# Kernel optimization log

Hardware: AMD Instinct MI355X
Metric: run time of the kernel (lower is better)

Reference implementation:

```python
import jax, jax.numpy as jnp
import numpy as np

EPS = float(np.finfo(np.float64).eps)  # matches np.finfo(float).eps in the torch code
NUM_SHARED, IN_DIM, NUM_OUT_CAPS, OUT_DIM = 32, 8, 10, 16
ROUTE_NUM = 3


def setup_inputs() -> dict:
    key = jax.random.key(0)
    k1, k2, k3 = jax.random.split(key, 3)
    bs, H, W = 256, 6, 6
    x = jax.random.normal(k1, (bs, NUM_SHARED * IN_DIM, H, W), jnp.float32)
    # grouped 1x1 conv weight, reshaped per group: (num_shared, num_out_caps*out_dim, in_dim)
    W_weight = jax.random.normal(k2, (NUM_SHARED, NUM_OUT_CAPS * OUT_DIM, IN_DIM), jnp.float32) * 0.05
    W_bias = jax.random.normal(k3, (NUM_SHARED * NUM_OUT_CAPS * OUT_DIM,), jnp.float32) * 0.05
    return {"x": x, "W_weight": W_weight, "W_bias": W_bias}


def reference(x, W_weight, W_bias):
    bs, C, H, Wd = x.shape
    G, KD, in_dim = W_weight.shape
    J, D = NUM_OUT_CAPS, OUT_DIM
    # grouped 1x1 conv == per-group matmul over channels
    xg = x.reshape(bs, G, in_dim, H * Wd)                     # b g i s
    pred = jnp.einsum('gki,bgis->bgks', W_weight, xg)
    pred = pred + W_bias.reshape(G, KD, 1)
    pred = pred.reshape(bs, G, J, D, H, Wd)
    pred = jnp.transpose(pred, (0, 2, 3, 1, 4, 5)).reshape(bs, J, D, G * H * Wd)  # b j d i
    I = G * H * Wd

    # dynamic routing
    b = jnp.zeros((bs, J, I), pred.dtype)
    v = None
    for it in range(ROUTE_NUM):
        c = jax.nn.softmax(b, axis=2)                          # b j i
        s = jnp.einsum('bjdi,bji->bjd', pred, c)               # b j d
        norm = jnp.linalg.norm(s, axis=2)                      # b j
        n2 = norm * norm
        coeff2 = (n2 / (1.0 + n2)) / (norm + EPS)              # squash, 'paper' manner
        v = s * coeff2[..., None]
        if it < ROUTE_NUM - 1:
            b = b + jnp.einsum('bjd,bjdi->bji', v, pred)
    return v
```

## Files before the change

kernel.cpp:

```cpp
#include <hip/hip_runtime.h>
#include <math.h>


#define G_    32
#define J_    10
#define D_    16
#define NT_   128
#define GSW_  148

__device__ __forceinline__ float dpp_add_x1(float v) {
    const int s = __builtin_amdgcn_update_dpp(0, __float_as_int(v), 0xB1, 0xF, 0xF, true);
    return v + __int_as_float(s);
}
__device__ __forceinline__ float dpp_add_x2(float v) {
    const int s = __builtin_amdgcn_update_dpp(0, __float_as_int(v), 0x4E, 0xF, 0xF, true);
    return v + __int_as_float(s);
}
__device__ __forceinline__ float dpp_x1(float v) {
    return __int_as_float(__builtin_amdgcn_update_dpp(0, __float_as_int(v), 0xB1, 0xF, 0xF, true));
}
__device__ __forceinline__ float dpp_x2(float v) {
    return __int_as_float(__builtin_amdgcn_update_dpp(0, __float_as_int(v), 0x4E, 0xF, 0xF, true));
}

__global__ __launch_bounds__(NT_) void caps_route_kernel(
    const float* __restrict__ x,
    const float* __restrict__ Wt,
    const float* __restrict__ bias,
    float* __restrict__ out)
{
    const int B = blockIdx.x, nwg = gridDim.x;
    const int bj = ((nwg & 7) == 0) ? (B & 7) * (nwg >> 3) + (B >> 3) : B;
    const int b = bj / J_, j = bj - b * J_;
    const int t = threadIdx.x;
    const int lane = t & 63, wid = t >> 6;
    const int g = t >> 2, c = t & 3;

    __shared__ float Wk[G_ * GSW_];
    __shared__ __align__(16) float swl[2][2][D_];
    __shared__ float esw[2][2];

    float xv[8][9];
    {
        const float* xb = x + (size_t)b * 9216 + (size_t)g * 288 + 4 * c;
        #pragma unroll
        for (int k = 0; k < 8; ++k) {
            const float4 a0 = *(const float4*)(xb + k * 36);
            const float4 a1 = *(const float4*)(xb + k * 36 + 16);
            xv[k][0] = a0.x; xv[k][1] = a0.y; xv[k][2] = a0.z; xv[k][3] = a0.w;
            xv[k][4] = a1.x; xv[k][5] = a1.y; xv[k][6] = a1.z; xv[k][7] = a1.w;
            xv[k][8] = xb[k * 36 + 32 - 3 * c];
        }
    }

    #pragma unroll
    for (int rr = 0; rr < 4; ++rr) {
        const int idx = t + rr * NT_;
        const int gg = idx >> 4, d = idx & 15;
        const float* src = Wt + (size_t)gg * 1280 + j * 128 + d * 8;
        const float4 a0 = *(const float4*)(src);
        const float4 a1 = *(const float4*)(src + 4);
        float* dst = Wk + gg * GSW_ + d;
        dst[0]   = a0.x; dst[16]  = a0.y; dst[32]  = a0.z; dst[48]  = a0.w;
        dst[64]  = a1.x; dst[80]  = a1.y; dst[96]  = a1.z; dst[112] = a1.w;
        dst[128] = bias[gg * 160 + j * 16 + d];
    }
    __syncthreads();

    float b_loc[9] = {0.f,0.f,0.f,0.f,0.f,0.f,0.f,0.f,0.f};
    const float EPS = 2.220446049250313e-16f;

    #pragma unroll 1
    for (int it = 0; it < 3; ++it) {
        const int kb = it & 1;

        float yp[8] = {0.f,0.f,0.f,0.f,0.f,0.f,0.f,0.f};
        float esum = 0.f;
        if (it == 0) {
            #pragma unroll
            for (int q = 0; q < 9; ++q) {
                #pragma unroll
                for (int k = 0; k < 8; ++k) yp[k] += xv[k][q];
            }
        } else {
            #pragma unroll
            for (int q = 0; q < 9; ++q) {
                const float e = __expf(b_loc[q]);
                esum += e;
                #pragma unroll
                for (int k = 0; k < 8; ++k) yp[k] += e * xv[k][q];
            }
        }
        #pragma unroll
        for (int k = 0; k < 8; ++k) {
            yp[k] = dpp_add_x1(yp[k]);
            yp[k] = dpp_add_x2(yp[k]);
        }
        if (it > 0) { esum = dpp_add_x1(esum); esum = dpp_add_x2(esum); }
        const float cg = (it == 0) ? 36.f : esum;

        float part[4];
        const float* wg = Wk + g * GSW_ + 4 * c;
        {
            const float4 wb = *(const float4*)(wg + 128);
            part[0] = wb.x * cg; part[1] = wb.y * cg;
            part[2] = wb.z * cg; part[3] = wb.w * cg;
            #pragma unroll
            for (int k = 0; k < 8; ++k) {
                const float4 wv = *(const float4*)(wg + k * 16);
                part[0] += wv.x * yp[k]; part[1] += wv.y * yp[k];
                part[2] += wv.z * yp[k]; part[3] += wv.w * yp[k];
            }
        }
        #pragma unroll
        for (int off = 4; off <= 32; off <<= 1) {
            #pragma unroll
            for (int m = 0; m < 4; ++m) part[m] += __shfl_xor(part[m], off);
            if (it > 0) esum += __shfl_xor(esum, off);
        }
        if (lane < 4) {
            float4 pw; pw.x = part[0]; pw.y = part[1]; pw.z = part[2]; pw.w = part[3];
            *(float4*)(&swl[kb][wid][4 * lane]) = pw;
            if (lane == 0) esw[kb][wid] = esum;
        }
        __syncthreads();

        const float denom = (it == 0) ? 1152.f : (esw[kb][0] + esw[kb][1]);

        if (it < 2) {
            float ssq = 0.f, ua = 0.f, ub = 0.f, u8v = 0.f;
            const float* wgc = Wk + g * GSW_;
            #pragma unroll
            for (int m = 0; m < 4; ++m) {
                const float4 sa = ((const float4*)swl[kb][0])[m];
                const float4 sb = ((const float4*)swl[kb][1])[m];
                float4 s4; s4.x = sa.x + sb.x; s4.y = sa.y + sb.y;
                           s4.z = sa.z + sb.z; s4.w = sa.w + sb.w;
                ssq += s4.x * s4.x + s4.y * s4.y + s4.z * s4.z + s4.w * s4.w;
                const float* wa = wgc + c * 16 + 4 * m;
                const float* wb = wgc + (c + 4) * 16 + 4 * m;
                const float* w8 = wgc + 128 + 4 * m;
                ua  += s4.x * wa[0] + s4.y * wa[1] + s4.z * wa[2] + s4.w * wa[3];
                ub  += s4.x * wb[0] + s4.y * wb[1] + s4.z * wb[2] + s4.w * wb[3];
                u8v += s4.x * w8[0] + s4.y * w8[1] + s4.z * w8[2] + s4.w * w8[3];
            }
            const float alpha = 1.f / denom;
            const float n2    = ssq * alpha * alpha;
            const float nrm   = sqrtf(n2);
            const float coeff = (n2 / (1.f + n2)) / (nrm + EPS);
            const float beta  = alpha * coeff;
            ua *= beta; ub *= beta; u8v *= beta;

            const float p1a = dpp_x1(ua);
            const float p1b = dpp_x1(ub);
            const bool  o1  = (c & 1) != 0;
            const float v0 = o1 ? p1a : ua;
            const float v1 = o1 ? ua  : p1a;
            const float v4 = o1 ? p1b : ub;
            const float v5 = o1 ? ub  : p1b;
            const float q0 = dpp_x2(v0);
            const float q1 = dpp_x2(v1);
            const float q4 = dpp_x2(v4);
            const float q5 = dpp_x2(v5);
            const bool  o2 = (c & 2) != 0;
            float uk[8];
            uk[0] = o2 ? q0 : v0;  uk[1] = o2 ? q1 : v1;
            uk[2] = o2 ? v0 : q0;  uk[3] = o2 ? v1 : q1;
            uk[4] = o2 ? q4 : v4;  uk[5] = o2 ? q5 : v5;
            uk[6] = o2 ? v4 : q4;  uk[7] = o2 ? v5 : q5;
            #pragma unroll
            for (int q = 0; q < 9; ++q) {
                float acc = u8v;
                #pragma unroll
                for (int k = 0; k < 8; ++k) acc += uk[k] * xv[k][q];
                b_loc[q] += acc;
            }
        } else {
            float ssq = 0.f;
            #pragma unroll
            for (int m = 0; m < 4; ++m) {
                const float4 sa = ((const float4*)swl[kb][0])[m];
                const float4 sb = ((const float4*)swl[kb][1])[m];
                const float sx = sa.x + sb.x, sy = sa.y + sb.y;
                const float sz = sa.z + sb.z, sw = sa.w + sb.w;
                ssq += sx * sx + sy * sy + sz * sz + sw * sw;
            }
            const float alpha = 1.f / denom;
            const float n2    = ssq * alpha * alpha;
            const float nrm   = sqrtf(n2);
            const float coeff = (n2 / (1.f + n2)) / (nrm + EPS);
            const float beta  = alpha * coeff;
            if (t < D_) {
                const float sd = swl[kb][0][t] + swl[kb][1][t];
                out[(size_t)bj * D_ + t] = sd * beta;
            }
        }
    }
}

extern "C" void kernel_launch(void* const* d_in, const int* in_sizes, int n_in,
                              void* d_out, int out_size, void* d_ws, size_t ws_size,
                              hipStream_t stream) {
    const float* x    = (const float*)d_in[0];
    const float* Wt   = (const float*)d_in[1];
    const float* bias = (const float*)d_in[2];
    float* out        = (float*)d_out;

    const int bs = in_sizes[0] / 9216;
    dim3 grid(bs * J_);
    dim3 block(NT_);
    caps_route_kernel<<<grid, block, 0, stream>>>(x, Wt, bias, out);
}
```

Measured before the change: 25.18 us.

## Keep per-thread weight slice in registers instead of staging in shared memory

Each thread now loads only its own 4x8 weight slice and 4 bias values straight into registers. This removes the shared-memory weight tile, its transposed staging writes and the initial __syncthreads. The back-projection of the squashed vector is rebuilt as per-thread partial dot products reduced over the 4 lanes of a group with DPP adds, replacing the earlier shared reads and DPP/select shuffles. The cost is about 36 more VGPRs per thread alongside the large x register array, which may lower occupancy.

Result: slower. 30.88 us (+22.6%).

```diff
diff --git a/kernel.cpp b/kernel.cpp
--- a/kernel.cpp
+++ b/kernel.cpp
@@ -6,7 +6,6 @@
 #define J_    10
 #define D_    16
 #define NT_   128
-#define GSW_  148
 
 __device__ __forceinline__ float dpp_add_x1(float v) {
     const int s = __builtin_amdgcn_update_dpp(0, __float_as_int(v), 0xB1, 0xF, 0xF, true);
@@ -15,12 +14,6 @@
 __device__ __forceinline__ float dpp_add_x2(float v) {
     const int s = __builtin_amdgcn_update_dpp(0, __float_as_int(v), 0x4E, 0xF, 0xF, true);
     return v + __int_as_float(s);
-}
-__device__ __forceinline__ float dpp_x1(float v) {
-    return __int_as_float(__builtin_amdgcn_update_dpp(0, __float_as_int(v), 0xB1, 0xF, 0xF, true));
-}
-__device__ __forceinline__ float dpp_x2(float v) {
-    return __int_as_float(__builtin_amdgcn_update_dpp(0, __float_as_int(v), 0x4E, 0xF, 0xF, true));
 }
 
 __global__ __launch_bounds__(NT_) void caps_route_kernel(
@@ -36,9 +29,23 @@
     const int lane = t & 63, wid = t >> 6;
     const int g = t >> 2, c = t & 3;
 
-    __shared__ float Wk[G_ * GSW_];
     __shared__ __align__(16) float swl[2][2][D_];
     __shared__ float esw[2][2];
+
+    float Wreg[4][8];
+    float br[4];
+    {
+        const float* wsrc = Wt + (size_t)g * 1280 + j * 128 + (4 * c) * 8;
+        #pragma unroll
+        for (int m = 0; m < 4; ++m) {
+            const float4 a0 = *(const float4*)(wsrc + m * 8);
+            const float4 a1 = *(const float4*)(wsrc + m * 8 + 4);
+            Wreg[m][0] = a0.x; Wreg[m][1] = a0.y; Wreg[m][2] = a0.z; Wreg[m][3] = a0.w;
+            Wreg[m][4] = a1.x; Wreg[m][5] = a1.y; Wreg[m][6] = a1.z; Wreg[m][7] = a1.w;
+        }
+        const float4 bb = *(const float4*)(bias + (size_t)g * 160 + j * 16 + 4 * c);
+        br[0] = bb.x; br[1] = bb.y; br[2] = bb.z; br[3] = bb.w;
+    }
 
     float xv[8][9];
     {
@@ -52,20 +59,6 @@
             xv[k][8] = xb[k * 36 + 32 - 3 * c];
         }
     }
-
-    #pragma unroll
-    for (int rr = 0; rr < 4; ++rr) {
-        const int idx = t + rr * NT_;
-        const int gg = idx >> 4, d = idx & 15;
-        const float* src = Wt + (size_t)gg * 1280 + j * 128 + d * 8;
-        const float4 a0 = *(const float4*)(src);
-        const float4 a1 = *(const float4*)(src + 4);
-        float* dst = Wk + gg * GSW_ + d;
-        dst[0]   = a0.x; dst[16]  = a0.y; dst[32]  = a0.z; dst[48]  = a0.w;
-        dst[64]  = a1.x; dst[80]  = a1.y; dst[96]  = a1.z; dst[112] = a1.w;
-        dst[128] = bias[gg * 160 + j * 16 + d];
-    }
-    __syncthreads();
 
     float b_loc[9] = {0.f,0.f,0.f,0.f,0.f,0.f,0.f,0.f,0.f};
     const float EPS = 2.220446049250313e-16f;
@@ -100,17 +93,12 @@
         const float cg = (it == 0) ? 36.f : esum;
 
         float part[4];
-        const float* wg = Wk + g * GSW_ + 4 * c;
-        {
-            const float4 wb = *(const float4*)(wg + 128);
-            part[0] = wb.x * cg; part[1] = wb.y * cg;
-            part[2] = wb.z * cg; part[3] = wb.w * cg;
+        #pragma unroll
+        for (int m = 0; m < 4; ++m) {
+            float p = br[m] * cg;
             #pragma unroll
-            for (int k = 0; k < 8; ++k) {
-                const float4 wv = *(const float4*)(wg + k * 16);
-                part[0] += wv.x * yp[k]; part[1] += wv.y * yp[k];
-                part[2] += wv.z * yp[k]; part[3] += wv.w * yp[k];
-            }
+            for (int k = 0; k < 8; ++k) p += Wreg[m][k] * yp[k];
+            part[m] = p;
         }
         #pragma unroll
         for (int off = 4; off <= 32; off <<= 1) {
@@ -127,69 +115,45 @@
 
         const float denom = (it == 0) ? 1152.f : (esw[kb][0] + esw[kb][1]);
 
+        const float4 sa = *(const float4*)(&swl[kb][0][4 * c]);
+        const float4 sb = *(const float4*)(&swl[kb][1][4 * c]);
+        float s4[4];
+        s4[0] = sa.x + sb.x; s4[1] = sa.y + sb.y;
+        s4[2] = sa.z + sb.z; s4[3] = sa.w + sb.w;
+
+        float ssq = s4[0]*s4[0] + s4[1]*s4[1] + s4[2]*s4[2] + s4[3]*s4[3];
+        ssq = dpp_add_x1(ssq);
+        ssq = dpp_add_x2(ssq);
+
+        const float alpha = 1.f / denom;
+        const float n2    = ssq * alpha * alpha;
+        const float nrm   = sqrtf(n2);
+        const float coeff = (n2 / (1.f + n2)) / (nrm + EPS);
+        const float beta  = alpha * coeff;
+
         if (it < 2) {
-            float ssq = 0.f, ua = 0.f, ub = 0.f, u8v = 0.f;
-            const float* wgc = Wk + g * GSW_;
+            const float t0 = s4[0] * beta, t1 = s4[1] * beta;
+            const float t2 = s4[2] * beta, t3 = s4[3] * beta;
+            float uk[8];
             #pragma unroll
-            for (int m = 0; m < 4; ++m) {
-                const float4 sa = ((const float4*)swl[kb][0])[m];
-                const float4 sb = ((const float4*)swl[kb][1])[m];
-                float4 s4; s4.x = sa.x + sb.x; s4.y = sa.y + sb.y;
-                           s4.z = sa.z + sb.z; s4.w = sa.w + sb.w;
-                ssq += s4.x * s4.x + s4.y * s4.y + s4.z * s4.z + s4.w * s4.w;
-                const float* wa = wgc + c * 16 + 4 * m;
-                const float* wb = wgc + (c + 4) * 16 + 4 * m;
-                const float* w8 = wgc + 128 + 4 * m;
-                ua  += s4.x * wa[0] + s4.y * wa[1] + s4.z * wa[2] + s4.w * wa[3];
-                ub  += s4.x * wb[0] + s4.y * wb[1] + s4.z * wb[2] + s4.w * wb[3];
-                u8v += s4.x * w8[0] + s4.y * w8[1] + s4.z * w8[2] + s4.w * w8[3];
+            for (int k = 0; k < 8; ++k) {
+                float uu = t0 * Wreg[0][k] + t1 * Wreg[1][k]
+                         + t2 * Wreg[2][k] + t3 * Wreg[3][k];
+                uu = dpp_add_x1(uu);
+                uk[k] = dpp_add_x2(uu);
             }
-            const float alpha = 1.f / denom;
-            const float n2    = ssq * alpha * alpha;
-            const float nrm   = sqrtf(n2);
-            const float coeff = (n2 / (1.f + n2)) / (nrm + EPS);
-            const float beta  = alpha * coeff;
-            ua *= beta; ub *= beta; u8v *= beta;
+            float u8 = t0 * br[0] + t1 * br[1] + t2 * br[2] + t3 * br[3];
+            u8 = dpp_add_x1(u8);
+            u8 = dpp_add_x2(u8);
 
-            const float p1a = dpp_x1(ua);
-            const float p1b = dpp_x1(ub);
-            const bool  o1  = (c & 1) != 0;
-            const float v0 = o1 ? p1a : ua;
-            const float v1 = o1 ? ua  : p1a;
-            const float v4 = o1 ? p1b : ub;
-            const float v5 = o1 ? ub  : p1b;
-            const float q0 = dpp_x2(v0);
-            const float q1 = dpp_x2(v1);
-            const float q4 = dpp_x2(v4);
-            const float q5 = dpp_x2(v5);
-            const bool  o2 = (c & 2) != 0;
-            float uk[8];
-            uk[0] = o2 ? q0 : v0;  uk[1] = o2 ? q1 : v1;
-            uk[2] = o2 ? v0 : q0;  uk[3] = o2 ? v1 : q1;
-            uk[4] = o2 ? q4 : v4;  uk[5] = o2 ? q5 : v5;
-            uk[6] = o2 ? v4 : q4;  uk[7] = o2 ? v5 : q5;
             #pragma unroll
             for (int q = 0; q < 9; ++q) {
-                float acc = u8v;
+                float acc = u8;
                 #pragma unroll
                 for (int k = 0; k < 8; ++k) acc += uk[k] * xv[k][q];
                 b_loc[q] += acc;
             }
         } else {
-            float ssq = 0.f;
-            #pragma unroll
-            for (int m = 0; m < 4; ++m) {
-                const float4 sa = ((const float4*)swl[kb][0])[m];
-                const float4 sb = ((const float4*)swl[kb][1])[m];
-                const float sx = sa.x + sb.x, sy = sa.y + sb.y;
-                const float sz = sa.z + sb.z, sw = sa.w + sb.w;
-                ssq += sx * sx + sy * sy + sz * sz + sw * sw;
-            }
-            const float alpha = 1.f / denom;
-            const float n2    = ssq * alpha * alpha;
-            const float nrm   = sqrtf(n2);
-            const float coeff = (n2 / (1.f + n2)) / (nrm + EPS);
-            const float beta  = alpha * coeff;
             if (t < D_) {
                 const float sd = swl[kb][0][t] + swl[kb][1][t];
                 out[(size_t)bj * D_ + t] = sd * beta;
```
